# Optimization experiments

Measured on AMD Instinct MI355X. Metric: run time of the kernel, lower is better.

The kernel has to match this reference:

```python
import jax, jax.numpy as jnp
import numpy as np

D_MODEL = 2048
N_HEADS = 16
GKV = 4
D_FF = 8192
D_HEAD = D_MODEL // N_HEADS
EPS = 1e-6


def rmsnorm(x, w):
    ms = jnp.mean(x * x, axis=-1, keepdims=True)
    return x * jax.lax.rsqrt(ms + EPS) * w


def attention(q, k, v, mask=None):
    # q: (B,Tq,H,d), k/v: (B,Tk,H,d)
    scale = 1.0 / jnp.sqrt(jnp.asarray(q.shape[-1], q.dtype))
    scores = jnp.einsum('bqhd,bkhd->bhqk', q, k) * scale
    if mask is not None:
        scores = scores + mask
    probs = jax.nn.softmax(scores, axis=-1)
    return jnp.einsum('bhqk,bkhd->bqhd', probs, v)


def setup_inputs() -> dict:
    key = jax.random.key(0)
    ks = jax.random.split(key, 12)
    B, T = 2, 2048
    s = 0.02
    return {
        'x': jax.random.normal(ks[0], (B, T, D_MODEL), jnp.float32),
        'k_ctx': jax.random.normal(ks[1], (B, T, GKV, D_HEAD), jnp.float32),
        'v_ctx': jax.random.normal(ks[2], (B, T, GKV, D_HEAD), jnp.float32),
        # cross-attn params (weights stored as (in, out); y = x @ W)
        'wq': jax.random.normal(ks[3], (D_MODEL, D_MODEL), jnp.float32) * s,
        'wo_cross': jax.random.normal(ks[4], (D_MODEL, D_MODEL), jnp.float32) * s,
        'norm_q_w': jnp.ones((D_MODEL,), jnp.float32),
        # self-attn params
        'wqkv': jax.random.normal(ks[5], (D_MODEL, 3 * D_MODEL), jnp.float32) * s,
        'wo_self': jax.random.normal(ks[6], (D_MODEL, D_MODEL), jnp.float32) * s,
        'norm_qkv_w': jnp.ones((D_MODEL,), jnp.float32),
        # FFN params (bias=False in FeedForward)
        'ffn_w1': jax.random.normal(ks[7], (D_MODEL, D_FF), jnp.float32) * s,
        'ffn_w2': jax.random.normal(ks[8], (D_FF, D_MODEL), jnp.float32) * s,
        'ffn_norm_w': jnp.ones((D_MODEL,), jnp.float32),
    }


def reference(x, k_ctx, v_ctx, wq, wo_cross, norm_q_w, wqkv, wo_self,
              norm_qkv_w, ffn_w1, ffn_w2, ffn_norm_w):
    B, T, D = x.shape
    repeat = N_HEADS // GKV

    # ---- cross attention (GQA) ----
    q = (rmsnorm(x, norm_q_w) @ wq).reshape(B, T, N_HEADS, D_HEAD)
    k = jnp.repeat(k_ctx, repeat, axis=2)  # (B,Tk,H,d), matches repeat_interleave
    v = jnp.repeat(v_ctx, repeat, axis=2)
    ctx = attention(q, k, v, mask=None).reshape(B, T, D)
    x = x + ctx @ wo_cross

    # ---- causal self attention ----
    xn = rmsnorm(x, norm_qkv_w)
    qkv = xn @ wqkv
    qs, ks_, vs = jnp.split(qkv, 3, axis=-1)
    qs = qs.reshape(B, T, N_HEADS, D_HEAD)
    ks_ = ks_.reshape(B, T, N_HEADS, D_HEAD)
    vs = vs.reshape(B, T, N_HEADS, D_HEAD)
    causal_mask = jnp.triu(jnp.full((T, T), -jnp.inf, x.dtype), k=1)[None, None]
    ctx2 = attention(qs, ks_, vs, mask=causal_mask).reshape(B, T, D)
    x = x + ctx2 @ wo_self

    # ---- FFN (SiLU) ----
    h = rmsnorm(x, ffn_norm_w)
    y = jax.nn.silu(h @ ffn_w1) @ ffn_w2
    return x + y
```

## Files before the change

kernel.cpp:

```cpp
#include <hip/hip_runtime.h>
#include <math.h>

typedef unsigned short u16;
typedef __attribute__((ext_vector_type(4))) u16 u16x4;
typedef __attribute__((ext_vector_type(8))) u16 u16x8;
typedef __attribute__((ext_vector_type(8))) __bf16 bf16x8;
typedef __attribute__((ext_vector_type(4))) float f32x4;
typedef __attribute__((ext_vector_type(16))) float f32x16;
typedef __attribute__((ext_vector_type(4))) unsigned u32x4;

#define D_MODEL 2048
#define SEQ 2048
#define BATCH 2
#define NH 16
#define HD 128
#define DFF 8192
#define ROWS (BATCH * SEQ)

__device__ __forceinline__ u16 f2bf(float f) {
  union { float f; unsigned u; } v; v.f = f;
  unsigned r = v.u + 0x7FFFu + ((v.u >> 16) & 1u);
  return (u16)(r >> 16);
}
__device__ __forceinline__ u16 to_bf16(float f) { return f2bf(f); }
__device__ __forceinline__ u16 to_bf16(u16 v) { return v; }

__device__ __forceinline__ f32x4 mfma16(u16x8 a, u16x8 b, f32x4 c) {
  return __builtin_amdgcn_mfma_f32_16x16x32_bf16(
      __builtin_bit_cast(bf16x8, a), __builtin_bit_cast(bf16x8, b), c, 0, 0, 0);
}
__device__ __forceinline__ f32x16 mfma32(u16x8 a, u16x8 b, f32x16 c) {
  return __builtin_amdgcn_mfma_f32_32x32x16_bf16(
      __builtin_bit_cast(bf16x8, a), __builtin_bit_cast(bf16x8, b), c, 0, 0, 0);
}

__device__ __forceinline__ void gll16(const void* g, void* l) {
  __builtin_amdgcn_global_load_lds(
      (const __attribute__((address_space(1))) void*)g,
      (__attribute__((address_space(3))) void*)l, 16, 0, 0);
}

__global__ __launch_bounds__(256) void cast_kernel(const float* __restrict__ in,
                                                   u16* __restrict__ out, int n8) {
  int i = blockIdx.x * 256 + threadIdx.x;
  if (i >= n8) return;
  const float4* p = (const float4*)in + (size_t)i * 2;
  float4 a = p[0], b = p[1];
  u16x8 o;
  o[0] = f2bf(a.x); o[1] = f2bf(a.y); o[2] = f2bf(a.z); o[3] = f2bf(a.w);
  o[4] = f2bf(b.x); o[5] = f2bf(b.y); o[6] = f2bf(b.z); o[7] = f2bf(b.w);
  *((u16x8*)out + i) = o;
}

__global__ __launch_bounds__(256) void cast_transpose_kernel(
    const float* __restrict__ in, u16* __restrict__ out, int K, int N) {
  __shared__ float tile[64][65];
  int n0 = blockIdx.x * 64, k0 = blockIdx.y * 64;
  int tx = threadIdx.x & 63, ty = threadIdx.x >> 6;
#pragma unroll
  for (int i = 0; i < 64; i += 4)
    tile[ty + i][tx] = in[(size_t)(k0 + ty + i) * N + n0 + tx];
  __syncthreads();
#pragma unroll
  for (int i = 0; i < 64; i += 4)
    out[(size_t)(n0 + ty + i) * K + k0 + tx] = f2bf(tile[tx][ty + i]);
}

template <typename ST>
__global__ __launch_bounds__(256) void build_vt_kernel(
    const ST* __restrict__ src, u16* __restrict__ dst, int HZ,
    size_t src_b_stride, size_t src_h_stride, int src_tok_stride) {
  __shared__ u16 tl[64][72];
  int z = blockIdx.z, zb = z / HZ, zh = z % HZ;
  const ST* s = src + (size_t)zb * src_b_stride + (size_t)zh * src_h_stride;
  int t0 = blockIdx.x * 64, d0 = blockIdx.y * 64;
  int rr = threadIdx.x >> 4, cc = (threadIdx.x & 15) * 4;
#pragma unroll
  for (int pp = 0; pp < 4; ++pp) {
    int t = pp * 16 + rr;
    const ST* sp = s + (size_t)(t0 + t) * src_tok_stride + d0 + cc;
#pragma unroll
    for (int j = 0; j < 4; ++j) tl[t][cc + j] = to_bf16(sp[j]);
  }
  __syncthreads();
  u16* dp = dst + (size_t)z * HD * SEQ;
#pragma unroll
  for (int pp = 0; pp < 4; ++pp) {
    int d = pp * 16 + rr;
    u16x4 w;
#pragma unroll
    for (int j = 0; j < 4; ++j) w[j] = tl[cc + j][d];
    *(u16x4*)(dp + (size_t)(d0 + d) * SEQ + t0 + cc) = w;
  }
}

__global__ __launch_bounds__(256) void rmsnorm_kernel(const float* __restrict__ x,
                                                      const float* __restrict__ w,
                                                      u16* __restrict__ out) {
  __shared__ float red[4];
  int row = blockIdx.x, t = threadIdx.x;
  const float4* xr = (const float4*)(x + (size_t)row * D_MODEL);
  float4 a = xr[t * 2], b = xr[t * 2 + 1];
  float ss = a.x * a.x + a.y * a.y + a.z * a.z + a.w * a.w +
             b.x * b.x + b.y * b.y + b.z * b.z + b.w * b.w;
#pragma unroll
  for (int m = 1; m < 64; m <<= 1) ss += __shfl_xor(ss, m, 64);
  if ((t & 63) == 0) red[t >> 6] = ss;
  __syncthreads();
  float tot = red[0] + red[1] + red[2] + red[3];
  float sc = rsqrtf(tot * (1.0f / D_MODEL) + 1e-6f);
  const float4* wr = (const float4*)w;
  float4 wa = wr[t * 2], wb = wr[t * 2 + 1];
  u16x8 o;
  o[0] = f2bf(a.x * sc * wa.x); o[1] = f2bf(a.y * sc * wa.y);
  o[2] = f2bf(a.z * sc * wa.z); o[3] = f2bf(a.w * sc * wa.w);
  o[4] = f2bf(b.x * sc * wb.x); o[5] = f2bf(b.y * sc * wb.y);
  o[6] = f2bf(b.z * sc * wb.z); o[7] = f2bf(b.w * sc * wb.w);
  *((u16x8*)(out + (size_t)row * D_MODEL) + t) = o;
}

template <int MODE>
__global__ __launch_bounds__(256) void combine_kernel(
    const float* __restrict__ p0, const float* __restrict__ p1,
    const float* __restrict__ res, void* __restrict__ outv, int n4) {
  int i = blockIdx.x * 256 + threadIdx.x;
  if (i >= n4) return;
  float4 a = ((const float4*)p0)[i];
  float4 b = ((const float4*)p1)[i];
  if (MODE == 1) {
    float4 r = ((const float4*)res)[i];
    float4 o;
    o.x = r.x + a.x + b.x; o.y = r.y + a.y + b.y;
    o.z = r.z + a.z + b.z; o.w = r.w + a.w + b.w;
    ((float4*)outv)[i] = o;
  } else {
    u16x4 o;
    o[0] = f2bf(a.x + b.x); o[1] = f2bf(a.y + b.y);
    o[2] = f2bf(a.z + b.z); o[3] = f2bf(a.w + b.w);
    ((u16x4*)outv)[i] = o;
  }
}

#define GPHASE(T, P, VM, ISSUE)                                                \
  {                                                                            \
    if (ISSUE) issue_half(4 * (T) + (P) + 4);                                  \
    asm volatile("s_waitcnt vmcnt(" #VM ")" ::: "memory");                     \
    __builtin_amdgcn_sched_barrier(0);                                         \
    __builtin_amdgcn_s_barrier();                                              \
    if (((P) & 1) == 0) {                                                      \
      const u16* SA = S + (((((T) & 1) << 2) | (((P) >> 1) << 1)) << 13);      \
      const u16* SB = SA + 8192;                                               \
      _Pragma("unroll") for (int m = 0; m < 8; ++m) {                          \
        int row = wm * 128 + m * 16 + r16;                                     \
        aF[m] = *(const u16x8*)(SA + row * 32 + ((kg ^ ((row >> 1) & 3)) << 3)); \
      }                                                                        \
      _Pragma("unroll") for (int n = 0; n < 4; ++n) {                          \
        int row = wn * 64 + n * 16 + r16;                                      \
        bF[n] = *(const u16x8*)(SB + row * 32 + ((kg ^ ((row >> 1) & 3)) << 3)); \
      }                                                                        \
    }                                                                          \
    __builtin_amdgcn_s_setprio(1);                                             \
    _Pragma("unroll") for (int m = 0; m < 8; ++m) {                            \
      acc[m][2 * ((P) & 1)] = mfma16(aF[m], bF[2 * ((P) & 1)], acc[m][2 * ((P) & 1)]); \
      acc[m][2 * ((P) & 1) + 1] =                                              \
          mfma16(aF[m], bF[2 * ((P) & 1) + 1], acc[m][2 * ((P) & 1) + 1]);     \
    }                                                                          \
    __builtin_amdgcn_s_setprio(0);                                             \
    __builtin_amdgcn_s_barrier();                                              \
  }

template <int EPI, int SPLIT>
__global__ __launch_bounds__(512, 1) void gemm256_kernel(
    const u16* __restrict__ A, const u16* __restrict__ Bt, void* __restrict__ Cv,
    float* __restrict__ Cv2, const float* __restrict__ res, int N, int K) {
  __shared__ __align__(16) u16 S[8 * 8192];
  const int tid = threadIdx.x, lane = tid & 63, wave = tid >> 6;
  const int wm = wave >> 2, wn = wave & 3;
  const int r16 = lane & 15, kg = lane >> 4;
  const int cols = N >> 8;
  const int cpx = gridDim.x >> 3;
  const int bid = blockIdx.x;
  const int swz = (bid & 7) * cpx + (bid >> 3);
  const int tiles = gridDim.x / SPLIT;
  const int tile = swz % tiles, kslice = swz / tiles;
  const int bm = (tile / cols) * 256, bn = (tile % cols) * 256;
  const int Ksub = K / SPLIT;
  const int koff = kslice * Ksub;
  const int nt = Ksub >> 6;

  auto issue_half = [&](int h) {
    int p = h & 3, t = h >> 2;
    const u16* src = (p & 1) ? (Bt + (size_t)bn * K) : (A + (size_t)bm * K);
    int kbase = koff + t * 64 + (p >> 1) * 32;
    u16* ldst = S + ((((t & 1) << 2) | p) << 13);
#pragma unroll
    for (int i = 0; i < 2; ++i) {
      int c = i * 512 + tid;
      int row = c >> 2, ch = c & 3;
      int kc = ch ^ ((row >> 1) & 3);
      gll16(src + (size_t)row * K + kbase + kc * 8, ldst + c * 8);
    }
  };

  u16x8 aF[8], bF[4];
  f32x4 acc[8][4] = {};

  issue_half(0); issue_half(1); issue_half(2); issue_half(3);
  for (int t = 0; t < nt - 1; ++t) {
    GPHASE(t, 0, 6, true);
    GPHASE(t, 1, 6, true);
    GPHASE(t, 2, 6, true);
    GPHASE(t, 3, 6, true);
  }
  {
    const int t = nt - 1;
    GPHASE(t, 0, 4, false);
    GPHASE(t, 1, 4, false);
    GPHASE(t, 2, 0, false);
    GPHASE(t, 3, 0, false);
  }

  float* Pp = (EPI == 3) ? (kslice ? Cv2 : (float*)Cv) : nullptr;
#pragma unroll
  for (int m = 0; m < 8; ++m) {
    int r0 = bm + wm * 128 + m * 16 + kg * 4;
#pragma unroll
    for (int n = 0; n < 4; ++n) {
      int cc = bn + wn * 64 + n * 16 + r16;
#pragma unroll
      for (int r = 0; r < 4; ++r) {
        size_t idx = (size_t)(r0 + r) * N + cc;
        float v = acc[m][n][r];
        if (EPI == 3) {
          Pp[idx] = v;
        } else if (EPI == 1) {
          ((float*)Cv)[idx] = res[idx] + v;
        } else if (EPI == 0) {
          ((u16*)Cv)[idx] = f2bf(v);
        } else {
          float s = v / (1.0f + __expf(-v));
          ((u16*)Cv)[idx] = f2bf(s);
        }
      }
    }
  }
}

#define NPHASE(T, P, VM, ISSUE)                                                \
  {                                                                            \
    if (ISSUE) issue_pair(2 * (T) + (P) + 2);                                  \
    asm volatile("s_waitcnt vmcnt(" #VM ")" ::: "memory");                     \
    __builtin_amdgcn_sched_barrier(0);                                         \
    __builtin_amdgcn_s_barrier();                                              \
    const u16* SA = S + ((((T) & 1) * 2 + (P)) * 12288);                       \
    const u16* SB = SA + 8192;                                                 \
    u16x8 aF[4], bF[4];                                                        \
    _Pragma("unroll") for (int m = 0; m < 4; ++m) {                            \
      int row = wm * 64 + m * 16 + r16;                                        \
      aF[m] = *(const u16x8*)(SA + row * 32 + ((kg ^ ((row >> 1) & 3)) << 3)); \
    }                                                                          \
    _Pragma("unroll") for (int n = 0; n < 4; ++n) {                            \
      int row = wn * 64 + n * 16 + r16;                                        \
      bF[n] = *(const u16x8*)(SB + row * 32 + ((kg ^ ((row >> 1) & 3)) << 3)); \
    }                                                                          \
    __builtin_amdgcn_s_setprio(1);                                             \
    _Pragma("unroll") for (int m = 0; m < 4; ++m)                              \
      _Pragma("unroll") for (int n = 0; n < 4; ++n)                            \
        acc[m][n] = mfma16(aF[m], bF[n], acc[m][n]);                           \
    __builtin_amdgcn_s_setprio(0);                                             \
    __builtin_amdgcn_s_barrier();                                              \
  }

template <int EPI>
__global__ __launch_bounds__(512, 1) void gemm_n128_kernel(
    const u16* __restrict__ A, const u16* __restrict__ Bt, void* __restrict__ Cv,
    const float* __restrict__ res, int N, int K) {
  __shared__ __align__(16) u16 S[4 * 12288];
  const int tid = threadIdx.x, lane = tid & 63, wave = tid >> 6;
  const int wm = wave >> 1, wn = wave & 1;
  const int r16 = lane & 15, kg = lane >> 4;
  const int cols = N >> 7;
  const int cpx = gridDim.x >> 3;
  const int bid = blockIdx.x;
  const int swz = (bid & 7) * cpx + (bid >> 3);
  const int bm = (swz / cols) * 256, bn = (swz % cols) * 128;
  const int nt = K >> 6;

  auto issue_pair = [&](int g) {
    int p = g & 1, t = g >> 1;
    int kbase = t * 64 + p * 32;
    u16* reg = S + (((t & 1) * 2 + p) * 12288);
#pragma unroll
    for (int i = 0; i < 2; ++i) {
      int c = i * 512 + tid;
      int row = c >> 2, ch = c & 3;
      int kc = ch ^ ((row >> 1) & 3);
      gll16(A + (size_t)(bm + row) * K + kbase + kc * 8, reg + c * 8);
    }
    {
      int row = tid >> 2, ch = tid & 3;
      int kc = ch ^ ((row >> 1) & 3);
      gll16(Bt + (size_t)(bn + row) * K + kbase + kc * 8, reg + 8192 + tid * 8);
    }
  };

  f32x4 acc[4][4] = {};

  issue_pair(0); issue_pair(1);
  for (int t = 0; t < nt - 1; ++t) {
    NPHASE(t, 0, 6, true);
    NPHASE(t, 1, 6, true);
  }
  {
    const int t = nt - 1;
    NPHASE(t, 0, 3, false);
    NPHASE(t, 1, 0, false);
  }

#pragma unroll
  for (int m = 0; m < 4; ++m) {
    int r0 = bm + wm * 64 + m * 16 + kg * 4;
#pragma unroll
    for (int n = 0; n < 4; ++n) {
      int cc = bn + wn * 64 + n * 16 + r16;
#pragma unroll
      for (int r = 0; r < 4; ++r) {
        size_t idx = (size_t)(r0 + r) * N + cc;
        float v = acc[m][n][r];
        if (EPI == 1) {
          ((float*)Cv)[idx] = res[idx] + v;
        } else if (EPI == 0) {
          ((u16*)Cv)[idx] = f2bf(v);
        } else {
          float s = v / (1.0f + __expf(-v));
          ((u16*)Cv)[idx] = f2bf(s);
        }
      }
    }
  }
}

template <bool CAUSAL, bool SELF>
__global__ __launch_bounds__(512, 2) void attn2_kernel(
    const u16* __restrict__ qp, const u16* __restrict__ kp,
    const u16* __restrict__ vtp, u16* __restrict__ outp) {
  __shared__ __align__(16) u16 Kl[64 * 128];
  __shared__ __align__(16) u16 Vl[128 * 64];
  const int tid = threadIdx.x, lane = tid & 63, wave = tid >> 6;
  const int lo = lane & 31, hi = lane >> 5;
  const int qt = blockIdx.x, bh = blockIdx.y, b = bh >> 4, h = bh & 15;
  const int qw0 = qt * 256 + wave * 32;
  const int qg = qw0 + lo;
  const size_t qstr = SELF ? 6144 : 2048;
  const size_t kstr = SELF ? 6144 : 512;
  const u16* qbase = qp + ((size_t)b * SEQ + qg) * qstr + h * HD;
  const u16* kbase = kp + (size_t)b * SEQ * kstr + (SELF ? (2048 + h * HD) : ((h >> 2) * HD));
  const u16* vbase = vtp + (size_t)(SELF ? (b * NH + h) : (b * 4 + (h >> 2))) * HD * SEQ;

  u16x8 qf[8];
#pragma unroll
  for (int dc = 0; dc < 8; ++dc) qf[dc] = *(const u16x8*)(qbase + dc * 16 + hi * 8);

  f32x16 o[4] = {};
  float m_run = -3e38f, l_run = 0.f;
  const int ntiles = CAUSAL ? qt * 4 + 4 : SEQ / 64;
  const float scale = 0.088388347648318447f;

  for (int kt = 0; kt < ntiles; ++kt) {
    __syncthreads();
#pragma unroll
    for (int i = 0; i < 2; ++i) {
      int c = i * 512 + tid;
      int krow = c >> 4, ks = c & 15;
      gll16(kbase + (size_t)(kt * 64 + krow) * kstr + ((ks ^ (krow & 15)) * 8),
            Kl + (size_t)c * 8);
      int vd = c >> 3, vs = c & 7;
      gll16(vbase + (size_t)vd * SEQ + kt * 64 + ((vs ^ (vd & 7)) * 8),
            Vl + (size_t)c * 8);
    }
    __syncthreads();
    if (CAUSAL && kt * 64 > qw0 + 31) continue;

    f32x16 s01[2] = {};
#pragma unroll
    for (int k2 = 0; k2 < 2; ++k2) {
      int key = k2 * 32 + lo;
#pragma unroll
      for (int mf = 0; mf < 8; ++mf) {
        int dc = mf * 2 + hi;
        u16x8 kf = *(const u16x8*)(Kl + key * 128 + ((dc ^ (key & 15)) * 8));
        s01[k2] = mfma32(kf, qf[mf], s01[k2]);
      }
    }

    float sv[32];
    float pm = -3e38f;
#pragma unroll
    for (int k2 = 0; k2 < 2; ++k2)
#pragma unroll
      for (int r = 0; r < 16; ++r) {
        float v = s01[k2][r];
        if (CAUSAL) {
          int key = kt * 64 + k2 * 32 + (r & 3) + 8 * (r >> 2) + 4 * hi;
          if (key > qg) v = -3e38f;
        }
        sv[k2 * 16 + r] = v;
        pm = fmaxf(pm, v);
      }
    pm = fmaxf(pm, __shfl_xor(pm, 32, 64));
    float mn = fmaxf(m_run, pm);
    float corr = __expf((m_run - mn) * scale);
    m_run = mn;

    float ps = 0.f;
    u16x8 pf[4];
#pragma unroll
    for (int k2 = 0; k2 < 2; ++k2)
#pragma unroll
      for (int hf = 0; hf < 2; ++hf) {
        float p8[8];
#pragma unroll
        for (int j = 0; j < 8; ++j) {
          p8[j] = __expf((sv[k2 * 16 + hf * 8 + j] - mn) * scale);
          ps += p8[j];
        }
        unsigned w0, w1, w2, w3;
        asm("v_cvt_pk_bf16_f32 %0, %1, %2" : "=v"(w0) : "v"(p8[0]), "v"(p8[1]));
        asm("v_cvt_pk_bf16_f32 %0, %1, %2" : "=v"(w1) : "v"(p8[2]), "v"(p8[3]));
        asm("v_cvt_pk_bf16_f32 %0, %1, %2" : "=v"(w2) : "v"(p8[4]), "v"(p8[5]));
        asm("v_cvt_pk_bf16_f32 %0, %1, %2" : "=v"(w3) : "v"(p8[6]), "v"(p8[7]));
        asm("v_permlane32_swap_b32 %0, %1" : "+v"(w0), "+v"(w2));
        asm("v_permlane32_swap_b32 %0, %1" : "+v"(w1), "+v"(w3));
        u32x4 fr; fr[0] = w0; fr[1] = w1; fr[2] = w2; fr[3] = w3;
        pf[k2 * 2 + hf] = __builtin_bit_cast(u16x8, fr);
      }
    ps += __shfl_xor(ps, 32, 64);
    l_run = l_run * corr + ps;

#pragma unroll
    for (int mb = 0; mb < 4; ++mb)
#pragma unroll
      for (int r = 0; r < 16; ++r) o[mb][r] *= corr;

#pragma unroll
    for (int kc = 0; kc < 4; ++kc) {
      int vcs = kc * 2 + hi;
#pragma unroll
      for (int mb = 0; mb < 4; ++mb) {
        int d = mb * 32 + lo;
        u16x8 vf = *(const u16x8*)(Vl + d * 64 + ((vcs ^ (d & 7)) * 8));
        o[mb] = mfma32(vf, pf[kc], o[mb]);
      }
    }
  }

  float inv = 1.0f / l_run;
  u16* ob = outp + ((size_t)b * SEQ + qg) * D_MODEL + h * HD + 4 * hi;
#pragma unroll
  for (int mb = 0; mb < 4; ++mb)
#pragma unroll
    for (int rq = 0; rq < 4; ++rq) {
      u16x4 w;
#pragma unroll
      for (int j = 0; j < 4; ++j) w[j] = f2bf(o[mb][rq * 4 + j] * inv);
      *(u16x4*)(ob + mb * 32 + rq * 8) = w;
    }
}

extern "C" void kernel_launch(void* const* d_in, const int* in_sizes, int n_in,
                              void* d_out, int out_size, void* d_ws, size_t ws_size,
                              hipStream_t stream) {
  const float* x          = (const float*)d_in[0];
  const float* k_ctx      = (const float*)d_in[1];
  const float* v_ctx      = (const float*)d_in[2];
  const float* wq         = (const float*)d_in[3];
  const float* wo_cross   = (const float*)d_in[4];
  const float* norm_q_w   = (const float*)d_in[5];
  const float* wqkv       = (const float*)d_in[6];
  const float* wo_self    = (const float*)d_in[7];
  const float* norm_qkv_w = (const float*)d_in[8];
  const float* ffn_w1     = (const float*)d_in[9];
  const float* ffn_w2     = (const float*)d_in[10];
  const float* ffn_norm_w = (const float*)d_in[11];
  float* out = (float*)d_out;

  char* ws = (char*)d_ws;
  size_t off = 0;
  auto alloc_u16 = [&](size_t n) { u16* p = (u16*)(ws + off); off += n * 2; return p; };
  auto alloc_f32 = [&](size_t n) { float* p = (float*)(ws + off); off += n * 4; return p; };
  u16* wq_bf   = alloc_u16((size_t)2048 * 2048);
  u16* woc_bf  = alloc_u16((size_t)2048 * 2048);
  u16* wqkv_bf = alloc_u16((size_t)2048 * 6144);
  u16* wos_bf  = alloc_u16((size_t)2048 * 2048);
  u16* w1_bf   = alloc_u16((size_t)2048 * 8192);
  u16* w2_bf   = alloc_u16((size_t)8192 * 2048);
  u16* xn_bf   = alloc_u16((size_t)ROWS * 2048);
  u16* qkv_bf  = alloc_u16((size_t)ROWS * 6144);
  u16* attn_bf = alloc_u16((size_t)ROWS * 2048);
  float* x1    = alloc_f32((size_t)ROWS * 2048);
  float* x2    = alloc_f32((size_t)ROWS * 2048);
  u16* q_bf    = qkv_bf;
  u16* h1_bf   = qkv_bf;
  u16* kc_bf   = (u16*)x2;
  u16* vt_ctx  = kc_bf + (size_t)BATCH * SEQ * 4 * HD;
  u16* vt_self = xn_bf;
  const int n4 = ROWS * 2048 / 4;

  auto castT = [&](const float* src, u16* dst, int K, int N) {
    cast_transpose_kernel<<<dim3(N / 64, K / 64), 256, 0, stream>>>(src, dst, K, N);
  };
  castT(wq, wq_bf, 2048, 2048);
  castT(wo_cross, woc_bf, 2048, 2048);
  castT(wqkv, wqkv_bf, 2048, 6144);
  castT(wo_self, wos_bf, 2048, 2048);
  castT(ffn_w1, w1_bf, 2048, 8192);
  castT(ffn_w2, w2_bf, 8192, 2048);
  {
    int n8 = (int)((size_t)BATCH * SEQ * 4 * HD / 8);
    cast_kernel<<<dim3((n8 + 255) / 256), dim3(256), 0, stream>>>(k_ctx, kc_bf, n8);
  }
  build_vt_kernel<float><<<dim3(SEQ / 64, HD / 64, BATCH * 4), 256, 0, stream>>>(
      v_ctx, vt_ctx, 4, (size_t)SEQ * 512, (size_t)HD, 512);

  rmsnorm_kernel<<<ROWS, 256, 0, stream>>>(x, norm_q_w, xn_bf);
  gemm_n128_kernel<0><<<dim3((ROWS / 256) * (2048 / 128)), 512, 0, stream>>>(
      xn_bf, wq_bf, q_bf, nullptr, 2048, 2048);
  attn2_kernel<false, false><<<dim3(SEQ / 256, BATCH * NH), 512, 0, stream>>>(
      q_bf, kc_bf, vt_ctx, attn_bf);
  gemm_n128_kernel<1><<<dim3((ROWS / 256) * (2048 / 128)), 512, 0, stream>>>(
      attn_bf, woc_bf, x1, x, 2048, 2048);

  rmsnorm_kernel<<<ROWS, 256, 0, stream>>>(x1, norm_qkv_w, xn_bf);
  gemm_n128_kernel<0><<<dim3((ROWS / 256) * (6144 / 128)), 512, 0, stream>>>(
      xn_bf, wqkv_bf, qkv_bf, nullptr, 6144, 2048);
  build_vt_kernel<u16><<<dim3(SEQ / 64, HD / 64, BATCH * NH), 256, 0, stream>>>(
      qkv_bf + 4096, vt_self, NH, (size_t)SEQ * 6144, (size_t)HD, 6144);
  attn2_kernel<true, true><<<dim3(SEQ / 256, BATCH * NH), 512, 0, stream>>>(
      qkv_bf, qkv_bf, vt_self, attn_bf);
  gemm_n128_kernel<1><<<dim3((ROWS / 256) * (2048 / 128)), 512, 0, stream>>>(
      attn_bf, wos_bf, x2, x1, 2048, 2048);

  rmsnorm_kernel<<<ROWS, 256, 0, stream>>>(x2, ffn_norm_w, xn_bf);
  gemm256_kernel<2, 1><<<dim3((ROWS / 256) * (8192 / 256)), 512, 0, stream>>>(
      xn_bf, w1_bf, h1_bf, nullptr, nullptr, 8192, 2048);
  gemm256_kernel<3, 2><<<dim3(256), 512, 0, stream>>>(
      h1_bf, w2_bf, out, x1, nullptr, 2048, 8192);
  combine_kernel<1><<<dim3((n4 + 255) / 256), 256, 0, stream>>>(
      out, x1, x2, out, n4);
}
```

Measured before the change: 838.0 us.

## Fuse V-transpose into QKV GEMM, halve GEMM LDS, defer softmax rescale

The QKV GEMM gets a new epilogue mode that writes the V columns straight into the transposed per-head layout, removing the separate build_vt launch. The vt_self buffer moves to x2, which is free at that point. The n128 GEMM drops from four to two LDS stages with one pair in flight, and launch bounds are raised to allow more blocks per CU. Attention skips the running-max update and output rescale when no lane's new max exceeds the old one by a threshold, saving the rescale multiplies. The trade-offs are less latency hiding in the GEMM and a bounded loss of exp headroom in the softmax.

```diff
diff --git a/kernel.cpp b/kernel.cpp
--- a/kernel.cpp
+++ b/kernel.cpp
@@ -246,13 +246,13 @@
   }
 }
 
-#define NPHASE(T, P, VM, ISSUE)                                                \
+#define NPH2(T, P, VM, ISSUE)                                                  \
   {                                                                            \
-    if (ISSUE) issue_pair(2 * (T) + (P) + 2);                                  \
+    if (ISSUE) issue_pair(2 * (T) + (P) + 1);                                  \
     asm volatile("s_waitcnt vmcnt(" #VM ")" ::: "memory");                     \
     __builtin_amdgcn_sched_barrier(0);                                         \
     __builtin_amdgcn_s_barrier();                                              \
-    const u16* SA = S + ((((T) & 1) * 2 + (P)) * 12288);                       \
+    const u16* SA = S + (((2 * (T) + (P)) & 1) * 12288);                       \
     const u16* SB = SA + 8192;                                                 \
     u16x8 aF[4], bF[4];                                                        \
     _Pragma("unroll") for (int m = 0; m < 4; ++m) {                            \
@@ -272,10 +272,10 @@
   }
 
 template <int EPI>
-__global__ __launch_bounds__(512, 1) void gemm_n128_kernel(
+__global__ __launch_bounds__(512, 4) void gemm_n128_kernel(
     const u16* __restrict__ A, const u16* __restrict__ Bt, void* __restrict__ Cv,
-    const float* __restrict__ res, int N, int K) {
-  __shared__ __align__(16) u16 S[4 * 12288];
+    const float* __restrict__ res, u16* __restrict__ vt, int N, int K) {
+  __shared__ __align__(16) u16 S[2 * 12288];
   const int tid = threadIdx.x, lane = tid & 63, wave = tid >> 6;
   const int wm = wave >> 1, wn = wave & 1;
   const int r16 = lane & 15, kg = lane >> 4;
@@ -289,7 +289,7 @@
   auto issue_pair = [&](int g) {
     int p = g & 1, t = g >> 1;
     int kbase = t * 64 + p * 32;
-    u16* reg = S + (((t & 1) * 2 + p) * 12288);
+    u16* reg = S + ((g & 1) * 12288);
 #pragma unroll
     for (int i = 0; i < 2; ++i) {
       int c = i * 512 + tid;
@@ -306,34 +306,40 @@
 
   f32x4 acc[4][4] = {};
 
-  issue_pair(0); issue_pair(1);
+  issue_pair(0);
   for (int t = 0; t < nt - 1; ++t) {
-    NPHASE(t, 0, 6, true);
-    NPHASE(t, 1, 6, true);
-  }
-  {
-    const int t = nt - 1;
-    NPHASE(t, 0, 3, false);
-    NPHASE(t, 1, 0, false);
-  }
-
+    NPH2(t, 0, 3, true);
+    NPH2(t, 1, 3, true);
+  }
+  NPH2(nt - 1, 0, 3, true);
+  NPH2(nt - 1, 1, 0, false);
+
+  const bool vmode = (EPI == 4) && (bn >= 4096);
 #pragma unroll
   for (int m = 0; m < 4; ++m) {
     int r0 = bm + wm * 64 + m * 16 + kg * 4;
 #pragma unroll
     for (int n = 0; n < 4; ++n) {
       int cc = bn + wn * 64 + n * 16 + r16;
-#pragma unroll
-      for (int r = 0; r < 4; ++r) {
-        size_t idx = (size_t)(r0 + r) * N + cc;
-        float v = acc[m][n][r];
-        if (EPI == 1) {
-          ((float*)Cv)[idx] = res[idx] + v;
-        } else if (EPI == 0) {
-          ((u16*)Cv)[idx] = f2bf(v);
-        } else {
-          float s = v / (1.0f + __expf(-v));
-          ((u16*)Cv)[idx] = f2bf(s);
+      if (vmode) {
+        int c2 = cc - 4096;
+        int z = (r0 >> 11) * NH + (c2 >> 7);
+        int d = c2 & 127;
+        int t0 = r0 & (SEQ - 1);
+        u16x4 w;
+#pragma unroll
+        for (int r = 0; r < 4; ++r) w[r] = f2bf(acc[m][n][r]);
+        *(u16x4*)(vt + ((size_t)z * HD + d) * SEQ + t0) = w;
+      } else {
+#pragma unroll
+        for (int r = 0; r < 4; ++r) {
+          size_t idx = (size_t)(r0 + r) * N + cc;
+          float v = acc[m][n][r];
+          if (EPI == 1) {
+            ((float*)Cv)[idx] = res[idx] + v;
+          } else {
+            ((u16*)Cv)[idx] = f2bf(v);
+          }
         }
       }
     }
@@ -365,6 +371,7 @@
   float m_run = -3e38f, l_run = 0.f;
   const int ntiles = CAUSAL ? qt * 4 + 4 : SEQ / 64;
   const float scale = 0.088388347648318447f;
+  const float defer_thr = 90.50966799187809f;
 
   for (int kt = 0; kt < ntiles; ++kt) {
     __syncthreads();
@@ -408,8 +415,10 @@
         pm = fmaxf(pm, v);
       }
     pm = fmaxf(pm, __shfl_xor(pm, 32, 64));
-    float mn = fmaxf(m_run, pm);
-    float corr = __expf((m_run - mn) * scale);
+
+    const bool defer = __all(pm - m_run <= defer_thr);
+    float mn = defer ? m_run : fmaxf(m_run, pm);
+    float corr = defer ? 1.0f : __expf((m_run - mn) * scale);
     m_run = mn;
 
     float ps = 0.f;
@@ -435,12 +444,16 @@
         pf[k2 * 2 + hf] = __builtin_bit_cast(u16x8, fr);
       }
     ps += __shfl_xor(ps, 32, 64);
-    l_run = l_run * corr + ps;
-
-#pragma unroll
-    for (int mb = 0; mb < 4; ++mb)
-#pragma unroll
-      for (int r = 0; r < 16; ++r) o[mb][r] *= corr;
+
+    if (defer) {
+      l_run += ps;
+    } else {
+      l_run = l_run * corr + ps;
+#pragma unroll
+      for (int mb = 0; mb < 4; ++mb)
+#pragma unroll
+        for (int r = 0; r < 16; ++r) o[mb][r] *= corr;
+    }
 
 #pragma unroll
     for (int kc = 0; kc < 4; ++kc) {
@@ -503,7 +516,7 @@
   u16* h1_bf   = qkv_bf;
   u16* kc_bf   = (u16*)x2;
   u16* vt_ctx  = kc_bf + (size_t)BATCH * SEQ * 4 * HD;
-  u16* vt_self = xn_bf;
+  u16* vt_self = (u16*)x2;
   const int n4 = ROWS * 2048 / 4;
 
   auto castT = [&](const float* src, u16* dst, int K, int N) {
@@ -524,21 +537,19 @@
 
   rmsnorm_kernel<<<ROWS, 256, 0, stream>>>(x, norm_q_w, xn_bf);
   gemm_n128_kernel<0><<<dim3((ROWS / 256) * (2048 / 128)), 512, 0, stream>>>(
-      xn_bf, wq_bf, q_bf, nullptr, 2048, 2048);
+      xn_bf, wq_bf, q_bf, nullptr, nullptr, 2048, 2048);
   attn2_kernel<false, false><<<dim3(SEQ / 256, BATCH * NH), 512, 0, stream>>>(
       q_bf, kc_bf, vt_ctx, attn_bf);
   gemm_n128_kernel<1><<<dim3((ROWS / 256) * (2048 / 128)), 512, 0, stream>>>(
-      attn_bf, woc_bf, x1, x, 2048, 2048);
+      attn_bf, woc_bf, x1, x, nullptr, 2048, 2048);
 
   rmsnorm_kernel<<<ROWS, 256, 0, stream>>>(x1, norm_qkv_w, xn_bf);
-  gemm_n128_kernel<0><<<dim3((ROWS / 256) * (6144 / 128)), 512, 0, stream>>>(
-      xn_bf, wqkv_bf, qkv_bf, nullptr, 6144, 2048);
-  build_vt_kernel<u16><<<dim3(SEQ / 64, HD / 64, BATCH * NH), 256, 0, stream>>>(
-      qkv_bf + 4096, vt_self, NH, (size_t)SEQ * 6144, (size_t)HD, 6144);
+  gemm_n128_kernel<4><<<dim3((ROWS / 256) * (6144 / 128)), 512, 0, stream>>>(
+      xn_bf, wqkv_bf, qkv_bf, nullptr, vt_self, 6144, 2048);
   attn2_kernel<true, true><<<dim3(SEQ / 256, BATCH * NH), 512, 0, stream>>>(
       qkv_bf, qkv_bf, vt_self, attn_bf);
   gemm_n128_kernel<1><<<dim3((ROWS / 256) * (2048 / 128)), 512, 0, stream>>>(
-      attn_bf, wos_bf, x2, x1, 2048, 2048);
+      attn_bf, wos_bf, x2, x1, nullptr, 2048, 2048);
 
   rmsnorm_kernel<<<ROWS, 256, 0, stream>>>(x2, ffn_norm_w, xn_bf);
   gemm256_kernel<2, 1><<<dim3((ROWS / 256) * (8192 / 256)), 512, 0, stream>>>(
```

Result: no change. 829.5 us (-1.0%).
